# Performance work log

Hardware: AMD Instinct MI355X
Metric: run time of the kernel (lower is better)

## Reference

```python
import jax, jax.numpy as jnp
import numpy as np

B, T, D, H, HD, FF = 1024, 128, 128, 4, 32, 512
SCALE = D ** -0.5  # NOTE: original scales by full EMBED_DIM**-0.5, not head_dim
EPS = 1e-5


def setup_inputs() -> dict:
    key = jax.random.key(0)
    ks = jax.random.split(key, 14)
    s = 0.02
    return {
        "x": jax.random.normal(ks[0], (B, T, D), dtype=jnp.float32),
        "ln1_g": jnp.ones((D,), jnp.float32),
        "ln1_b": jnp.zeros((D,), jnp.float32),
        "Wq": jax.random.normal(ks[1], (H, HD, D), jnp.float32) * s,
        "Wk": jax.random.normal(ks[2], (H, HD, D), jnp.float32) * s,
        "Wv": jax.random.normal(ks[3], (H, HD, D), jnp.float32) * s,
        "Wo": jax.random.normal(ks[4], (D, D), jnp.float32) * s,
        "bo": jnp.zeros((D,), jnp.float32),
        "ln2_g": jnp.ones((D,), jnp.float32),
        "ln2_b": jnp.zeros((D,), jnp.float32),
        "W1": jax.random.normal(ks[5], (FF, D), jnp.float32) * s,
        "b1": jnp.zeros((FF,), jnp.float32),
        "W2": jax.random.normal(ks[6], (D, FF), jnp.float32) * s,
        "b2": jnp.zeros((D,), jnp.float32),
    }


def _layer_norm(x, g, b):
    mu = jnp.mean(x, axis=-1, keepdims=True)
    var = jnp.mean(jnp.square(x - mu), axis=-1, keepdims=True)
    return (x - mu) * jax.lax.rsqrt(var + EPS) * g + b


def reference(x, ln1_g, ln1_b, Wq, Wk, Wv, Wo, bo, ln2_g, ln2_b, W1, b1, W2, b2):
    # --- attention sub-block ---
    h = _layer_norm(x, ln1_g, ln1_b)                       # [B,T,D]
    q = jnp.einsum('btd,nhd->bnth', h, Wq)                 # [B,H,T,HD]
    k = jnp.einsum('btd,nhd->bnth', h, Wk)
    v = jnp.einsum('btd,nhd->bnth', h, Wv)
    scores = jnp.einsum('bnth,bnsh->bnts', q, k) * SCALE   # [B,H,T,T]
    causal = jnp.tril(jnp.ones((T, T), dtype=bool))
    scores = jnp.where(causal, scores, -jnp.inf)
    w = jax.nn.softmax(scores, axis=-1)                    # dropout = eval identity
    attn = jnp.einsum('bnts,bnsh->bnth', w, v)             # [B,H,T,HD]
    attn = attn.transpose(0, 2, 1, 3).reshape(B, T, D)     # concat heads
    x = x + attn @ Wo.T + bo
    # --- feed-forward sub-block ---
    h2 = _layer_norm(x, ln2_g, ln2_b)
    ff = jax.nn.relu(h2 @ W1.T + b1) @ W2.T + b2
    return x + ff
```

## Files before the change

kernel.cpp:

```cpp
#include <hip/hip_runtime.h>
#include <hip/hip_bf16.h>


typedef short bf16x8 __attribute__((ext_vector_type(8)));
typedef float f32x4  __attribute__((ext_vector_type(4)));
typedef unsigned short u16;
typedef unsigned int   u32;

#define TT   128
#define DDIM 128
#define FFD  512
#define PIT  136

__device__ __forceinline__ u16 f2b(float f) {
    __hip_bfloat16 h = __float2bfloat16(f);
    return __builtin_bit_cast(u16, h);
}
__device__ __forceinline__ bf16x8 ldfrag(const u16* p) {
    return __builtin_bit_cast(bf16x8, *reinterpret_cast<const uint4*>(p));
}
__device__ __forceinline__ bf16x8 ldfrag_f32(const float* p) {
    float4 a = *reinterpret_cast<const float4*>(p);
    float4 b = *reinterpret_cast<const float4*>(p + 4);
    bf16x8 r;
    r[0] = (short)f2b(a.x); r[1] = (short)f2b(a.y);
    r[2] = (short)f2b(a.z); r[3] = (short)f2b(a.w);
    r[4] = (short)f2b(b.x); r[5] = (short)f2b(b.y);
    r[6] = (short)f2b(b.z); r[7] = (short)f2b(b.w);
    return r;
}
__device__ __forceinline__ f32x4 mfma16(bf16x8 a, bf16x8 b, f32x4 c) {
    return __builtin_amdgcn_mfma_f32_16x16x32_bf16(a, b, c, 0, 0, 0);
}

__global__ __launch_bounds__(512, 2) void tblock_kernel(
    const float* __restrict__ x,
    const float* __restrict__ ln1g, const float* __restrict__ ln1b,
    const float* __restrict__ Wq,   const float* __restrict__ Wk, const float* __restrict__ Wv,
    const float* __restrict__ Wo,   const float* __restrict__ bo,
    const float* __restrict__ ln2g, const float* __restrict__ ln2b,
    const float* __restrict__ W1,   const float* __restrict__ b1,
    const float* __restrict__ W2,   const float* __restrict__ b2,
    float* __restrict__ out)
{
    __shared__ __align__(16) u16 sm[4 * TT * PIT];
    u16* bufA = sm;
    u16* bufB = sm + 1 * TT * PIT;
    u16* bufC = sm + 2 * TT * PIT;
    u16* bufD = sm + 3 * TT * PIT;

    const int b    = blockIdx.x;
    const int tid  = threadIdx.x;
    const int w    = tid >> 6;
    const int l    = tid & 63;
    const int lq   = l & 15;
    const int quad = l >> 4;
    const float* xb = x + (size_t)b * (TT * DDIM);

    {
        const int row = tid >> 2, part = tid & 3;
        const float* src = xb + row * DDIM + part * 32;
        float v[32];
        float s = 0.f, s2 = 0.f;
        #pragma unroll
        for (int i = 0; i < 8; i++) {
            float4 u = *reinterpret_cast<const float4*>(src + i * 4);
            v[i * 4 + 0] = u.x; v[i * 4 + 1] = u.y;
            v[i * 4 + 2] = u.z; v[i * 4 + 3] = u.w;
            s  += u.x + u.y + u.z + u.w;
            s2 += u.x * u.x + u.y * u.y + u.z * u.z + u.w * u.w;
        }
        s  += __shfl_xor(s, 1);  s2 += __shfl_xor(s2, 1);
        s  += __shfl_xor(s, 2);  s2 += __shfl_xor(s2, 2);
        float mean = s * (1.f / 128.f);
        float var  = fmaxf(s2 * (1.f / 128.f) - mean * mean, 0.f);
        float rstd = rsqrtf(var + 1e-5f);
        u16* dst = bufA + row * PIT + part * 32;
        #pragma unroll
        for (int i = 0; i < 4; i++) {
            u32 o4[4];
            #pragma unroll
            for (int j = 0; j < 4; j++) {
                int c = part * 32 + i * 8 + 2 * j;
                float r0 = (v[i * 8 + 2 * j]     - mean) * rstd * ln1g[c]     + ln1b[c];
                float r1 = (v[i * 8 + 2 * j + 1] - mean) * rstd * ln1g[c + 1] + ln1b[c + 1];
                o4[j] = (u32)f2b(r0) | ((u32)f2b(r1) << 16);
            }
            uint4 pk; pk.x = o4[0]; pk.y = o4[1]; pk.z = o4[2]; pk.w = o4[3];
            *reinterpret_cast<uint4*>(dst + i * 8) = pk;
        }
    }
    __syncthreads();

    {
        bf16x8 bq[4], bk[4];
        #pragma unroll
        for (int ks = 0; ks < 4; ks++) {
            bq[ks] = ldfrag_f32(Wq + (w * 16 + lq) * DDIM + ks * 32 + quad * 8);
            bk[ks] = ldfrag_f32(Wk + (w * 16 + lq) * DDIM + ks * 32 + quad * 8);
        }
        #pragma unroll
        for (int m = 0; m < 8; m++) {
            f32x4 accq = {0, 0, 0, 0}, acck = {0, 0, 0, 0};
            #pragma unroll
            for (int ks = 0; ks < 4; ks++) {
                bf16x8 a = ldfrag(bufA + (m * 16 + lq) * PIT + ks * 32 + quad * 8);
                accq = mfma16(a, bq[ks], accq);
                acck = mfma16(a, bk[ks], acck);
            }
            #pragma unroll
            for (int r = 0; r < 4; r++) {
                int t = m * 16 + quad * 4 + r;
                bufB[t * PIT + w * 16 + lq] = f2b(accq[r]);
                bufC[t * PIT + w * 16 + lq] = f2b(acck[r]);
            }
        }
        bf16x8 av[4];
        #pragma unroll
        for (int ks = 0; ks < 4; ks++)
            av[ks] = ldfrag_f32(Wv + (w * 16 + lq) * DDIM + ks * 32 + quad * 8);
        #pragma unroll
        for (int n = 0; n < 8; n++) {
            f32x4 acc = {0, 0, 0, 0};
            #pragma unroll
            for (int ks = 0; ks < 4; ks++) {
                bf16x8 bh = ldfrag(bufA + (n * 16 + lq) * PIT + ks * 32 + quad * 8);
                acc = mfma16(av[ks], bh, acc);
            }
            #pragma unroll
            for (int r = 0; r < 4; r++) {
                int o = w * 16 + quad * 4 + r;
                bufD[o * PIT + n * 16 + lq] = f2b(acc[r]);
            }
        }
    }
    __syncthreads();

    const float SCALE = 0.08838834764831845f;
    #pragma unroll 1
    for (int h = 0; h < 4; h++) {
        bf16x8 aq = ldfrag(bufB + (w * 16 + lq) * PIT + h * 32 + quad * 8);
        float p[8][4];
        #pragma unroll
        for (int n = 0; n < 8; n++) {
            bf16x8 bk = ldfrag(bufC + (n * 16 + lq) * PIT + h * 32 + quad * 8);
            f32x4 s4 = {0, 0, 0, 0};
            s4 = mfma16(aq, bk, s4);
            #pragma unroll
            for (int r = 0; r < 4; r++) p[n][r] = s4[r];
        }
        #pragma unroll
        for (int r = 0; r < 4; r++) {
            int t = w * 16 + quad * 4 + r;
            float mx = -3.0e38f;
            #pragma unroll
            for (int n = 0; n < 8; n++) {
                int sc = n * 16 + lq;
                float val = p[n][r] * SCALE;
                p[n][r] = val;
                mx = (sc <= t) ? fmaxf(mx, val) : mx;
            }
            mx = fmaxf(mx, __shfl_xor(mx, 1));
            mx = fmaxf(mx, __shfl_xor(mx, 2));
            mx = fmaxf(mx, __shfl_xor(mx, 4));
            mx = fmaxf(mx, __shfl_xor(mx, 8));
            float sum = 0.f;
            #pragma unroll
            for (int n = 0; n < 8; n++) {
                int sc = n * 16 + lq;
                float e = (sc <= t) ? __expf(p[n][r] - mx) : 0.f;
                p[n][r] = e; sum += e;
            }
            sum += __shfl_xor(sum, 1);
            sum += __shfl_xor(sum, 2);
            sum += __shfl_xor(sum, 4);
            sum += __shfl_xor(sum, 8);
            float inv = 1.f / sum;
            #pragma unroll
            for (int n = 0; n < 8; n++)
                bufA[t * PIT + n * 16 + lq] = f2b(p[n][r] * inv);
        }
        asm volatile("s_waitcnt lgkmcnt(0)" ::: "memory");
        __builtin_amdgcn_sched_barrier(0);
        f32x4 o0 = {0, 0, 0, 0}, o1 = {0, 0, 0, 0};
        #pragma unroll
        for (int ks = 0; ks < 4; ks++) {
            bf16x8 ap  = ldfrag(bufA + (w * 16 + lq) * PIT + ks * 32 + quad * 8);
            bf16x8 bv0 = ldfrag(bufD + (h * 32 + lq) * PIT + ks * 32 + quad * 8);
            bf16x8 bv1 = ldfrag(bufD + (h * 32 + 16 + lq) * PIT + ks * 32 + quad * 8);
            o0 = mfma16(ap, bv0, o0);
            o1 = mfma16(ap, bv1, o1);
        }
        #pragma unroll
        for (int r = 0; r < 4; r++) {
            int t = w * 16 + quad * 4 + r;
            bufB[t * PIT + h * 32 + lq]      = f2b(o0[r]);
            bufB[t * PIT + h * 32 + 16 + lq] = f2b(o1[r]);
        }
    }
    __syncthreads();

    float x1res[8][4];
    const int dcol = w * 16 + lq;
    {
        bf16x8 bw[4];
        #pragma unroll
        for (int ks = 0; ks < 4; ks++)
            bw[ks] = ldfrag_f32(Wo + (w * 16 + lq) * DDIM + ks * 32 + quad * 8);
        const float bov = bo[dcol];
        #pragma unroll
        for (int m = 0; m < 8; m++) {
            f32x4 acc = {0, 0, 0, 0};
            #pragma unroll
            for (int ks = 0; ks < 4; ks++) {
                bf16x8 a = ldfrag(bufB + (m * 16 + lq) * PIT + ks * 32 + quad * 8);
                acc = mfma16(a, bw[ks], acc);
            }
            #pragma unroll
            for (int r = 0; r < 4; r++) {
                int t = m * 16 + quad * 4 + r;
                float xv = xb[t * DDIM + dcol];
                float x1 = acc[r] + xv + bov;
                x1res[m][r] = x1;
                bufC[t * PIT + dcol] = f2b(x1);
            }
        }
    }
    __syncthreads();

    {
        const int row = tid >> 2, part = tid & 3;
        const u16* src = bufC + row * PIT + part * 32;
        float v[32];
        float s = 0.f, s2 = 0.f;
        #pragma unroll
        for (int i = 0; i < 4; i++) {
            uint4 u = *reinterpret_cast<const uint4*>(src + i * 8);
            u32 arr[4] = {u.x, u.y, u.z, u.w};
            #pragma unroll
            for (int j = 0; j < 4; j++) {
                float f0 = __uint_as_float((arr[j] & 0xffffu) << 16);
                float f1 = __uint_as_float(arr[j] & 0xffff0000u);
                v[i * 8 + 2 * j] = f0; v[i * 8 + 2 * j + 1] = f1;
                s += f0 + f1; s2 += f0 * f0 + f1 * f1;
            }
        }
        s  += __shfl_xor(s, 1);  s2 += __shfl_xor(s2, 1);
        s  += __shfl_xor(s, 2);  s2 += __shfl_xor(s2, 2);
        float mean = s * (1.f / 128.f);
        float var  = fmaxf(s2 * (1.f / 128.f) - mean * mean, 0.f);
        float rstd = rsqrtf(var + 1e-5f);
        u16* dst = bufD + row * PIT + part * 32;
        #pragma unroll
        for (int i = 0; i < 4; i++) {
            u32 o4[4];
            #pragma unroll
            for (int j = 0; j < 4; j++) {
                int c = part * 32 + i * 8 + 2 * j;
                float r0 = (v[i * 8 + 2 * j]     - mean) * rstd * ln2g[c]     + ln2b[c];
                float r1 = (v[i * 8 + 2 * j + 1] - mean) * rstd * ln2g[c + 1] + ln2b[c + 1];
                o4[j] = (u32)f2b(r0) | ((u32)f2b(r1) << 16);
            }
            uint4 pk; pk.x = o4[0]; pk.y = o4[1]; pk.z = o4[2]; pk.w = o4[3];
            *reinterpret_cast<uint4*>(dst + i * 8) = pk;
        }
    }
    __syncthreads();

    f32x4 oacc[8];
    #pragma unroll
    for (int m = 0; m < 8; m++) oacc[m] = f32x4{0, 0, 0, 0};

    #pragma unroll 1
    for (int fc = 0; fc < 4; fc++) {
        const int fbase = fc * 128;
        u16* gbuf = (fc & 1) ? bufB : bufA;
        bf16x8 wf1[4];
        #pragma unroll
        for (int ks = 0; ks < 4; ks++)
            wf1[ks] = ldfrag_f32(W1 + (fbase + w * 16 + lq) * DDIM + ks * 32 + quad * 8);
        const float b1v = b1[fbase + w * 16 + lq];
        #pragma unroll
        for (int m = 0; m < 8; m++) {
            f32x4 acc = {0, 0, 0, 0};
            #pragma unroll
            for (int ks = 0; ks < 4; ks++) {
                bf16x8 a = ldfrag(bufD + (m * 16 + lq) * PIT + ks * 32 + quad * 8);
                acc = mfma16(a, wf1[ks], acc);
            }
            #pragma unroll
            for (int r = 0; r < 4; r++) {
                int t = m * 16 + quad * 4 + r;
                float g = acc[r] + b1v;
                g = g > 0.f ? g : 0.f;
                gbuf[t * PIT + w * 16 + lq] = f2b(g);
            }
        }
        __syncthreads();
        bf16x8 wf2[4];
        #pragma unroll
        for (int ks = 0; ks < 4; ks++)
            wf2[ks] = ldfrag_f32(W2 + (w * 16 + lq) * FFD + fbase + ks * 32 + quad * 8);
        #pragma unroll
        for (int m = 0; m < 8; m++) {
            #pragma unroll
            for (int ks = 0; ks < 4; ks++) {
                bf16x8 a = ldfrag(gbuf + (m * 16 + lq) * PIT + ks * 32 + quad * 8);
                oacc[m] = mfma16(a, wf2[ks], oacc[m]);
            }
        }
    }

    {
        const float b2v = b2[dcol];
        float* ob = out + (size_t)b * (TT * DDIM);
        #pragma unroll
        for (int m = 0; m < 8; m++) {
            #pragma unroll
            for (int r = 0; r < 4; r++) {
                int t = m * 16 + quad * 4 + r;
                ob[t * DDIM + dcol] = oacc[m][r] + x1res[m][r] + b2v;
            }
        }
    }
}

extern "C" void kernel_launch(void* const* d_in, const int* in_sizes, int n_in,
                              void* d_out, int out_size, void* d_ws, size_t ws_size,
                              hipStream_t stream) {
    const float* x    = (const float*)d_in[0];
    const float* ln1g = (const float*)d_in[1];
    const float* ln1b = (const float*)d_in[2];
    const float* Wq   = (const float*)d_in[3];
    const float* Wk   = (const float*)d_in[4];
    const float* Wv   = (const float*)d_in[5];
    const float* Wo   = (const float*)d_in[6];
    const float* bo   = (const float*)d_in[7];
    const float* ln2g = (const float*)d_in[8];
    const float* ln2b = (const float*)d_in[9];
    const float* W1   = (const float*)d_in[10];
    const float* b1   = (const float*)d_in[11];
    const float* W2   = (const float*)d_in[12];
    const float* b2   = (const float*)d_in[13];
    float* out = (float*)d_out;

    const int nblocks = in_sizes[0] / (TT * DDIM);
    tblock_kernel<<<dim3(nblocks), dim3(512), 0, stream>>>(
        x, ln1g, ln1b, Wq, Wk, Wv, Wo, bo, ln2g, ln2b, W1, b1, W2, b2, out);
}
```

Baseline: 319.1 us.

## Swap MFMA operand order for transposed accumulators and vectorized packed stores

Swaps the A/B operands of every MFMA so each lane's four accumulator values lie along the contiguous feature dimension. Scalar bf16 LDS stores and scalar global loads and stores then become packed 64-bit LDS stores and float4 global accesses. Softmax now reduces across lanes with xor 16/32 shuffles, uses exp2 with log2(e) folded into the scale, and applies the 1/sum after the PV product instead of before. This cuts LDS store instructions and shuffle count, at the cost of rounding unnormalized probabilities to bf16.

```diff
diff --git a/kernel.cpp b/kernel.cpp
--- a/kernel.cpp
+++ b/kernel.cpp
@@ -12,9 +12,28 @@
 #define FFD  512
 #define PIT  136
 
+#define QSC 0.12751744f
+
+#if defined(__has_builtin)
+#if __has_builtin(__builtin_amdgcn_exp2f)
+#define EXP2F(x) __builtin_amdgcn_exp2f(x)
+#else
+#define EXP2F(x) exp2f(x)
+#endif
+#else
+#define EXP2F(x) exp2f(x)
+#endif
+
 __device__ __forceinline__ u16 f2b(float f) {
     __hip_bfloat16 h = __float2bfloat16(f);
     return __builtin_bit_cast(u16, h);
+}
+__device__ __forceinline__ u32 pk2(float x, float y) {
+    return (u32)f2b(x) | ((u32)f2b(y) << 16);
+}
+__device__ __forceinline__ void st_b64(u16* p, u32 lo, u32 hi) {
+    uint2 v; v.x = lo; v.y = hi;
+    *reinterpret_cast<uint2*>(p) = v;
 }
 __device__ __forceinline__ bf16x8 ldfrag(const u16* p) {
     return __builtin_bit_cast(bf16x8, *reinterpret_cast<const uint4*>(p));
@@ -93,27 +112,24 @@
     __syncthreads();
 
     {
-        bf16x8 bq[4], bk[4];
+        bf16x8 aq[4], ak[4];
         #pragma unroll
         for (int ks = 0; ks < 4; ks++) {
-            bq[ks] = ldfrag_f32(Wq + (w * 16 + lq) * DDIM + ks * 32 + quad * 8);
-            bk[ks] = ldfrag_f32(Wk + (w * 16 + lq) * DDIM + ks * 32 + quad * 8);
+            aq[ks] = ldfrag_f32(Wq + (w * 16 + lq) * DDIM + ks * 32 + quad * 8);
+            ak[ks] = ldfrag_f32(Wk + (w * 16 + lq) * DDIM + ks * 32 + quad * 8);
         }
         #pragma unroll
         for (int m = 0; m < 8; m++) {
             f32x4 accq = {0, 0, 0, 0}, acck = {0, 0, 0, 0};
             #pragma unroll
             for (int ks = 0; ks < 4; ks++) {
-                bf16x8 a = ldfrag(bufA + (m * 16 + lq) * PIT + ks * 32 + quad * 8);
-                accq = mfma16(a, bq[ks], accq);
-                acck = mfma16(a, bk[ks], acck);
-            }
-            #pragma unroll
-            for (int r = 0; r < 4; r++) {
-                int t = m * 16 + quad * 4 + r;
-                bufB[t * PIT + w * 16 + lq] = f2b(accq[r]);
-                bufC[t * PIT + w * 16 + lq] = f2b(acck[r]);
-            }
+                bf16x8 bh = ldfrag(bufA + (m * 16 + lq) * PIT + ks * 32 + quad * 8);
+                accq = mfma16(aq[ks], bh, accq);
+                acck = mfma16(ak[ks], bh, acck);
+            }
+            int t = m * 16 + lq;
+            st_b64(bufB + t * PIT + w * 16 + quad * 4, pk2(accq[0], accq[1]), pk2(accq[2], accq[3]));
+            st_b64(bufC + t * PIT + w * 16 + quad * 4, pk2(acck[0], acck[1]), pk2(acck[2], acck[3]));
         }
         bf16x8 av[4];
         #pragma unroll
@@ -136,94 +152,87 @@
     }
     __syncthreads();
 
-    const float SCALE = 0.08838834764831845f;
+    const int trow = w * 16 + lq;
     #pragma unroll 1
     for (int h = 0; h < 4; h++) {
-        bf16x8 aq = ldfrag(bufB + (w * 16 + lq) * PIT + h * 32 + quad * 8);
+        bf16x8 qb = ldfrag(bufB + trow * PIT + h * 32 + quad * 8);
         float p[8][4];
         #pragma unroll
         for (int n = 0; n < 8; n++) {
-            bf16x8 bk = ldfrag(bufC + (n * 16 + lq) * PIT + h * 32 + quad * 8);
-            f32x4 s4 = {0, 0, 0, 0};
-            s4 = mfma16(aq, bk, s4);
+            bf16x8 ka = ldfrag(bufC + (n * 16 + lq) * PIT + h * 32 + quad * 8);
+            f32x4 s4 = mfma16(ka, qb, f32x4{0, 0, 0, 0});
             #pragma unroll
             for (int r = 0; r < 4; r++) p[n][r] = s4[r];
         }
-        #pragma unroll
-        for (int r = 0; r < 4; r++) {
-            int t = w * 16 + quad * 4 + r;
-            float mx = -3.0e38f;
-            #pragma unroll
-            for (int n = 0; n < 8; n++) {
-                int sc = n * 16 + lq;
-                float val = p[n][r] * SCALE;
-                p[n][r] = val;
-                mx = (sc <= t) ? fmaxf(mx, val) : mx;
-            }
-            mx = fmaxf(mx, __shfl_xor(mx, 1));
-            mx = fmaxf(mx, __shfl_xor(mx, 2));
-            mx = fmaxf(mx, __shfl_xor(mx, 4));
-            mx = fmaxf(mx, __shfl_xor(mx, 8));
-            float sum = 0.f;
-            #pragma unroll
-            for (int n = 0; n < 8; n++) {
-                int sc = n * 16 + lq;
-                float e = (sc <= t) ? __expf(p[n][r] - mx) : 0.f;
-                p[n][r] = e; sum += e;
-            }
-            sum += __shfl_xor(sum, 1);
-            sum += __shfl_xor(sum, 2);
-            sum += __shfl_xor(sum, 4);
-            sum += __shfl_xor(sum, 8);
-            float inv = 1.f / sum;
-            #pragma unroll
-            for (int n = 0; n < 8; n++)
-                bufA[t * PIT + n * 16 + lq] = f2b(p[n][r] * inv);
-        }
+        float mx = -3.0e38f;
+        #pragma unroll
+        for (int n = 0; n < 8; n++) {
+            #pragma unroll
+            for (int r = 0; r < 4; r++) {
+                int sc = n * 16 + quad * 4 + r;
+                float q = p[n][r] * QSC;
+                p[n][r] = q;
+                mx = (sc <= trow) ? fmaxf(mx, q) : mx;
+            }
+        }
+        mx = fmaxf(mx, __shfl_xor(mx, 16));
+        mx = fmaxf(mx, __shfl_xor(mx, 32));
+        float sum = 0.f;
+        #pragma unroll
+        for (int n = 0; n < 8; n++) {
+            float e[4];
+            #pragma unroll
+            for (int r = 0; r < 4; r++) {
+                int sc = n * 16 + quad * 4 + r;
+                e[r] = (sc <= trow) ? EXP2F(p[n][r] - mx) : 0.f;
+                sum += e[r];
+            }
+            st_b64(bufA + trow * PIT + n * 16 + quad * 4, pk2(e[0], e[1]), pk2(e[2], e[3]));
+        }
+        sum += __shfl_xor(sum, 16);
+        sum += __shfl_xor(sum, 32);
+        float inv = 1.f / sum;
         asm volatile("s_waitcnt lgkmcnt(0)" ::: "memory");
         __builtin_amdgcn_sched_barrier(0);
         f32x4 o0 = {0, 0, 0, 0}, o1 = {0, 0, 0, 0};
         #pragma unroll
         for (int ks = 0; ks < 4; ks++) {
-            bf16x8 ap  = ldfrag(bufA + (w * 16 + lq) * PIT + ks * 32 + quad * 8);
-            bf16x8 bv0 = ldfrag(bufD + (h * 32 + lq) * PIT + ks * 32 + quad * 8);
-            bf16x8 bv1 = ldfrag(bufD + (h * 32 + 16 + lq) * PIT + ks * 32 + quad * 8);
-            o0 = mfma16(ap, bv0, o0);
-            o1 = mfma16(ap, bv1, o1);
-        }
-        #pragma unroll
-        for (int r = 0; r < 4; r++) {
-            int t = w * 16 + quad * 4 + r;
-            bufB[t * PIT + h * 32 + lq]      = f2b(o0[r]);
-            bufB[t * PIT + h * 32 + 16 + lq] = f2b(o1[r]);
-        }
+            bf16x8 pb  = ldfrag(bufA + trow * PIT + ks * 32 + quad * 8);
+            bf16x8 va0 = ldfrag(bufD + (h * 32 + lq) * PIT + ks * 32 + quad * 8);
+            bf16x8 va1 = ldfrag(bufD + (h * 32 + 16 + lq) * PIT + ks * 32 + quad * 8);
+            o0 = mfma16(va0, pb, o0);
+            o1 = mfma16(va1, pb, o1);
+        }
+        #pragma unroll
+        for (int r = 0; r < 4; r++) { o0[r] *= inv; o1[r] *= inv; }
+        st_b64(bufB + trow * PIT + h * 32 + quad * 4,      pk2(o0[0], o0[1]), pk2(o0[2], o0[3]));
+        st_b64(bufB + trow * PIT + h * 32 + 16 + quad * 4, pk2(o1[0], o1[1]), pk2(o1[2], o1[3]));
     }
     __syncthreads();
 
     float x1res[8][4];
-    const int dcol = w * 16 + lq;
-    {
-        bf16x8 bw[4];
+    {
+        bf16x8 woa[4];
         #pragma unroll
         for (int ks = 0; ks < 4; ks++)
-            bw[ks] = ldfrag_f32(Wo + (w * 16 + lq) * DDIM + ks * 32 + quad * 8);
-        const float bov = bo[dcol];
+            woa[ks] = ldfrag_f32(Wo + (w * 16 + lq) * DDIM + ks * 32 + quad * 8);
+        const float4 bo4 = *reinterpret_cast<const float4*>(bo + w * 16 + quad * 4);
         #pragma unroll
         for (int m = 0; m < 8; m++) {
             f32x4 acc = {0, 0, 0, 0};
             #pragma unroll
             for (int ks = 0; ks < 4; ks++) {
-                bf16x8 a = ldfrag(bufB + (m * 16 + lq) * PIT + ks * 32 + quad * 8);
-                acc = mfma16(a, bw[ks], acc);
-            }
-            #pragma unroll
-            for (int r = 0; r < 4; r++) {
-                int t = m * 16 + quad * 4 + r;
-                float xv = xb[t * DDIM + dcol];
-                float x1 = acc[r] + xv + bov;
-                x1res[m][r] = x1;
-                bufC[t * PIT + dcol] = f2b(x1);
-            }
+                bf16x8 ab = ldfrag(bufB + (m * 16 + lq) * PIT + ks * 32 + quad * 8);
+                acc = mfma16(woa[ks], ab, acc);
+            }
+            int t = m * 16 + lq;
+            const float4 xv = *reinterpret_cast<const float4*>(xb + t * DDIM + w * 16 + quad * 4);
+            float v0 = acc[0] + xv.x + bo4.x;
+            float v1 = acc[1] + xv.y + bo4.y;
+            float v2 = acc[2] + xv.z + bo4.z;
+            float v3 = acc[3] + xv.w + bo4.w;
+            x1res[m][0] = v0; x1res[m][1] = v1; x1res[m][2] = v2; x1res[m][3] = v3;
+            st_b64(bufC + t * PIT + w * 16 + quad * 4, pk2(v0, v1), pk2(v2, v3));
         }
     }
     __syncthreads();
@@ -275,52 +284,53 @@
     for (int fc = 0; fc < 4; fc++) {
         const int fbase = fc * 128;
         u16* gbuf = (fc & 1) ? bufB : bufA;
-        bf16x8 wf1[4];
+        bf16x8 w1a[4];
         #pragma unroll
         for (int ks = 0; ks < 4; ks++)
-            wf1[ks] = ldfrag_f32(W1 + (fbase + w * 16 + lq) * DDIM + ks * 32 + quad * 8);
-        const float b1v = b1[fbase + w * 16 + lq];
+            w1a[ks] = ldfrag_f32(W1 + (fbase + w * 16 + lq) * DDIM + ks * 32 + quad * 8);
+        const float4 b14 = *reinterpret_cast<const float4*>(b1 + fbase + w * 16 + quad * 4);
         #pragma unroll
         for (int m = 0; m < 8; m++) {
             f32x4 acc = {0, 0, 0, 0};
             #pragma unroll
             for (int ks = 0; ks < 4; ks++) {
-                bf16x8 a = ldfrag(bufD + (m * 16 + lq) * PIT + ks * 32 + quad * 8);
-                acc = mfma16(a, wf1[ks], acc);
-            }
-            #pragma unroll
-            for (int r = 0; r < 4; r++) {
-                int t = m * 16 + quad * 4 + r;
-                float g = acc[r] + b1v;
-                g = g > 0.f ? g : 0.f;
-                gbuf[t * PIT + w * 16 + lq] = f2b(g);
-            }
+                bf16x8 hb = ldfrag(bufD + (m * 16 + lq) * PIT + ks * 32 + quad * 8);
+                acc = mfma16(w1a[ks], hb, acc);
+            }
+            int t = m * 16 + lq;
+            float g0 = fmaxf(acc[0] + b14.x, 0.f);
+            float g1 = fmaxf(acc[1] + b14.y, 0.f);
+            float g2 = fmaxf(acc[2] + b14.z, 0.f);
+            float g3 = fmaxf(acc[3] + b14.w, 0.f);
+            st_b64(gbuf + t * PIT + w * 16 + quad * 4, pk2(g0, g1), pk2(g2, g3));
         }
         __syncthreads();
-        bf16x8 wf2[4];
+        bf16x8 w2a[4];
         #pragma unroll
         for (int ks = 0; ks < 4; ks++)
-            wf2[ks] = ldfrag_f32(W2 + (w * 16 + lq) * FFD + fbase + ks * 32 + quad * 8);
-        #pragma unroll
-        for (int m = 0; m < 8; m++) {
-            #pragma unroll
-            for (int ks = 0; ks < 4; ks++) {
-                bf16x8 a = ldfrag(gbuf + (m * 16 + lq) * PIT + ks * 32 + quad * 8);
-                oacc[m] = mfma16(a, wf2[ks], oacc[m]);
-            }
-        }
-    }
-
-    {
-        const float b2v = b2[dcol];
+            w2a[ks] = ldfrag_f32(W2 + (w * 16 + lq) * FFD + fbase + ks * 32 + quad * 8);
+        #pragma unroll
+        for (int m = 0; m < 8; m++) {
+            #pragma unroll
+            for (int ks = 0; ks < 4; ks++) {
+                bf16x8 gb = ldfrag(gbuf + (m * 16 + lq) * PIT + ks * 32 + quad * 8);
+                oacc[m] = mfma16(w2a[ks], gb, oacc[m]);
+            }
+        }
+    }
+
+    {
+        const float4 b24 = *reinterpret_cast<const float4*>(b2 + w * 16 + quad * 4);
         float* ob = out + (size_t)b * (TT * DDIM);
         #pragma unroll
         for (int m = 0; m < 8; m++) {
-            #pragma unroll
-            for (int r = 0; r < 4; r++) {
-                int t = m * 16 + quad * 4 + r;
-                ob[t * DDIM + dcol] = oacc[m][r] + x1res[m][r] + b2v;
-            }
+            int t = m * 16 + lq;
+            float4 o;
+            o.x = oacc[m][0] + x1res[m][0] + b24.x;
+            o.y = oacc[m][1] + x1res[m][1] + b24.y;
+            o.z = oacc[m][2] + x1res[m][2] + b24.z;
+            o.w = oacc[m][3] + x1res[m][3] + b24.w;
+            *reinterpret_cast<float4*>(ob + t * DDIM + w * 16 + quad * 4) = o;
         }
     }
 }
```

Measured after the change: 312.8 us. -2.0%, faster.
